# Kernel optimization log

Hardware: AMD Instinct MI355X
Metric: run time of the kernel (lower is better)

Reference implementation:

```python
import jax, jax.numpy as jnp
import numpy as np
import math

R1 = 1.0
R2 = 4.0
NBINS_XY = 4
NBINS_ZY = 4
PARTITIONS = NBINS_XY * NBINS_ZY * 2  # 32
TOPK = 200
TWO_PI = 2.0 * math.pi
PI = math.pi


def setup_inputs() -> dict:
    key = jax.random.key(0)
    k1, k2 = jax.random.split(key)
    # LiDAR-like coordinates, ~[-30, 30] meters
    sampled_vehicle_points = jax.random.normal(k1, (1024, 3), dtype=jnp.float32) * 20.0
    fusion_point = jax.random.normal(k2, (20000, 3), dtype=jnp.float32) * 20.0
    return {"sampled_vehicle_points": sampled_vehicle_points, "fusion_point": fusion_point}


def _compute_partitions_batch(q):
    # q: [S, K, 3]. rel[b, i, j] = q[b, j] - q[b, i]  (A.unsqueeze(1) - B.unsqueeze(2))
    rel = q[:, None, :, :] - q[:, :, None, :]  # [S, K, K, 3]
    angles_xy = jnp.fmod(jnp.arctan2(rel[..., 1], rel[..., 0]) + TWO_PI, TWO_PI)
    angles_zy = jnp.fmod(jnp.arctan2(rel[..., 1], rel[..., 2]) + TWO_PI, PI)
    xy_bins = jnp.floor(angles_xy / (TWO_PI / NBINS_XY))
    zy_bins = jnp.floor(angles_zy / (PI / NBINS_ZY))
    # hash(A, B, seed=NBINS_ZY): -1 where either < 0
    angle_ok = (xy_bins >= 0) & (zy_bins >= 0)
    angles_bins = jnp.where(angle_ok, xy_bins * NBINS_ZY + zy_bins, -1.0)
    D = jnp.sqrt(jnp.sum(rel * rel, axis=-1) + 1e-7)  # [S, K, K]
    dist_bins = jnp.where(D >= R2, 1.0, jnp.where(D >= R1, 0.0, -1.0))
    bin_ok = (dist_bins >= 0) & (angles_bins >= 0)
    bins = jnp.where(bin_ok, dist_bins * (NBINS_XY * NBINS_ZY) + angles_bins, -1.0)
    return bins  # [S, K, K] float, -1 for ignored


def reference(sampled_vehicle_points, fusion_point):
    # kNN query: K nearest fusion points for each sampled vehicle point
    d2 = jnp.sum(
        (sampled_vehicle_points[:, None, :] - fusion_point[None, :, :]) ** 2, axis=-1
    )  # [S, Nf]
    _, idx = jax.lax.top_k(-d2, TOPK)  # indices of TOPK smallest distances
    queried = fusion_point[idx]  # [S, K, 3]

    bins = _compute_partitions_batch(queried)  # [S, K, K]
    row0 = bins[:, 0, :]  # [S, K] — only row 0 is used by the loss
    # points_in_partition[s, p] = sum_j (row0[s, j] == p) + 1
    counts = jnp.sum(
        row0[:, :, None] == jnp.arange(PARTITIONS, dtype=bins.dtype)[None, None, :],
        axis=1,
    ).astype(jnp.float32) + 1.0  # [S, P]
    pip = counts / jnp.linalg.norm(counts, axis=-1, keepdims=True) * 4.0
    gt_dist = jax.nn.softmax(pip, axis=-1)
    return gt_dist
```

## Files before the change

kernel.cpp:

```cpp
#include <hip/hip_runtime.h>
#include <math.h>

#define KTOP 200
#define NPART 32
#define BLOCK 512
#define NHIST 2048
#define CAND_CAP 512
#define WCAP 512
#define CLIST_CAP 1536
#define SRANK_MIN 64u

__device__ __forceinline__ float d2_ref(float ax, float ay, float az,
                                        float bx, float by, float bz) {
    float dx = __fsub_rn(ax, bx), dy = __fsub_rn(ay, by), dz = __fsub_rn(az, bz);
    return __fadd_rn(__fadd_rn(__fmul_rn(dx, dx), __fmul_rn(dy, dy)), __fmul_rn(dz, dz));
}

__device__ __forceinline__ unsigned key_of(const float* __restrict__ fus, int j,
                                           float vx, float vy, float vz) {
    return __float_as_uint(d2_ref(vx, vy, vz, fus[3*j], fus[3*j+1], fus[3*j+2]));
}

__device__ __forceinline__ int compute_bin(float rx, float ry, float rz) {
    const float TWO_PI_F = (float)6.283185307179586;
    const float PI_F     = (float)3.141592653589793;
    const float XY_W     = (float)(6.283185307179586 / 4.0);
    const float ZY_W     = (float)(3.141592653589793 / 4.0);

    float d2 = __fadd_rn(__fadd_rn(__fmul_rn(rx, rx), __fmul_rn(ry, ry)), __fmul_rn(rz, rz));
    float D  = sqrtf(__fadd_rn(d2, 1e-7f));
    float dist_bin;
    if (D >= 4.0f)      dist_bin = 1.0f;
    else if (D >= 1.0f) dist_bin = 0.0f;
    else                return -1;

    float axy = fmodf(atan2f(ry, rx) + TWO_PI_F, TWO_PI_F);
    float azy = fmodf(atan2f(ry, rz) + TWO_PI_F, PI_F);
    float xyb = floorf(__fdiv_rn(axy, XY_W));
    float zyb = floorf(__fdiv_rn(azy, ZY_W));
    if (!(xyb >= 0.0f && zyb >= 0.0f)) return -1;
    float ab  = xyb * 4.0f + zyb;
    int bin = (int)(dist_bin * 16.0f + ab);
    return bin;
}

__global__ __launch_bounds__(BLOCK, 8)
void shape_context_kernel(const float* __restrict__ veh,
                          const float* __restrict__ fus,
                          float* __restrict__ out,
                          int nfus) {
    const int b   = blockIdx.x;
    const int tid = threadIdx.x;
    const int lane = tid & 63;
    const int wid  = tid >> 6;

    __shared__ unsigned int hist[NHIST];
    __shared__ unsigned long long clist[CLIST_CAP];
    __shared__ unsigned long long cand[CAND_CAP];
    __shared__ int wlist[WCAP];
    __shared__ unsigned int hist32[NPART];
    __shared__ unsigned int waveTot[BLOCK / 64];
    __shared__ unsigned int waveBase[BLOCK / 64];
    __shared__ unsigned int s_bucket, s_rem, s_bcount;
    __shared__ int s_candCount, s_wcount, s_clistCount;
    __shared__ float s_q0[3];
    __shared__ unsigned long long s_minPacked, s_lowBound;

    const float vx = veh[b * 3 + 0], vy = veh[b * 3 + 1], vz = veh[b * 3 + 2];
    const float4* fus4 = (const float4*)fus;
    const int ntrip = nfus >> 2;

    if (tid == 0) { s_minPacked = ~0ull; s_candCount = 0; s_wcount = 0; s_clistCount = 0; }
    for (int i = tid; i < NHIST; i += BLOCK) hist[i] = 0;
    if (tid < NPART) hist32[tid] = 0;
    __syncthreads();

    auto find_bucket = [&](unsigned remq) {
        if (tid == 0) s_bucket = 0xFFFFFFFFu;
        const int PER = NHIST / BLOCK;
        int base = tid * PER;
        unsigned p = 0;
        #pragma unroll
        for (int i = 0; i < PER; i++) p += hist[base + i];
        unsigned incl = p;
        #pragma unroll
        for (int d = 1; d < 64; d <<= 1) {
            unsigned n = __shfl_up(incl, d, 64);
            if (lane >= d) incl += n;
        }
        if (lane == 63) waveTot[wid] = incl;
        __syncthreads();
        if (tid == 0) {
            unsigned acc = 0;
            for (int w = 0; w < BLOCK / 64; w++) { waveBase[w] = acc; acc += waveTot[w]; }
        }
        __syncthreads();
        unsigned excl = waveBase[wid] + incl - p;
        if (excl < remq && remq <= excl + p) {
            unsigned cum = excl;
            #pragma unroll
            for (int i = 0; i < PER; i++) {
                unsigned c = hist[base + i];
                if (cum + c >= remq) { s_bucket = base + i; s_rem = remq - cum; s_bcount = c; break; }
                cum += c;
            }
        }
        __syncthreads();
    };

    auto push_l = [&](unsigned k, unsigned j) {
        int pos = atomicAdd(&s_clistCount, 1);
        if (pos < CLIST_CAP) clist[pos] = ((unsigned long long)k << 32) | j;
    };

    unsigned k0 = 0, k1 = 0, k2 = 0, k3 = 0;
    const bool t0v = (tid < ntrip);
    if (t0v) {
        float4 A = fus4[3 * tid], Bq = fus4[3 * tid + 1], Cq = fus4[3 * tid + 2];
        k0 = __float_as_uint(d2_ref(vx, vy, vz, A.x,  A.y,  A.z));
        k1 = __float_as_uint(d2_ref(vx, vy, vz, A.w,  Bq.x, Bq.y));
        k2 = __float_as_uint(d2_ref(vx, vy, vz, Bq.z, Bq.w, Cq.x));
        k3 = __float_as_uint(d2_ref(vx, vy, vz, Cq.y, Cq.z, Cq.w));
        atomicAdd(&hist[k0 >> 21], 1u);
        atomicAdd(&hist[k1 >> 21], 1u);
        atomicAdd(&hist[k2 >> 21], 1u);
        atomicAdd(&hist[k3 >> 21], 1u);
    }
    __syncthreads();

    unsigned srank;
    {
        long long sample = (long long)((ntrip < BLOCK) ? ntrip : BLOCK) * 4;
        if (sample >= (long long)nfus) {
            srank = KTOP;
        } else {
            unsigned s2 = (unsigned)(((long long)3 * KTOP * sample + nfus - 1) / nfus);
            srank = (s2 < SRANK_MIN) ? SRANK_MIN : s2;
        }
    }
    find_bucket(srank);
    const unsigned E = (s_bucket < NHIST) ? s_bucket : (NHIST - 1);
    const unsigned maxKey = ((E + 1u) << 21) - 1u;

    if (t0v) {
        unsigned jb = 4u * (unsigned)tid;
        if (k0 <= maxKey) push_l(k0, jb + 0);
        if (k1 <= maxKey) push_l(k1, jb + 1);
        if (k2 <= maxKey) push_l(k2, jb + 2);
        if (k3 <= maxKey) push_l(k3, jb + 3);
    }

    {
        int m = BLOCK + tid;
        bool valid = (m < ntrip);
        float4 A, Bq, Cq;
        if (valid) { A = fus4[3 * m]; Bq = fus4[3 * m + 1]; Cq = fus4[3 * m + 2]; }
        while (valid) {
            const int mn = m + BLOCK;
            const bool vnext = (mn < ntrip);
            float4 An, Bn, Cn;
            if (vnext) { An = fus4[3 * mn]; Bn = fus4[3 * mn + 1]; Cn = fus4[3 * mn + 2]; }

            unsigned q0k = __float_as_uint(d2_ref(vx, vy, vz, A.x,  A.y,  A.z));
            unsigned q1k = __float_as_uint(d2_ref(vx, vy, vz, A.w,  Bq.x, Bq.y));
            unsigned q2k = __float_as_uint(d2_ref(vx, vy, vz, Bq.z, Bq.w, Cq.x));
            unsigned q3k = __float_as_uint(d2_ref(vx, vy, vz, Cq.y, Cq.z, Cq.w));
            unsigned long long m0 = __ballot(q0k <= maxKey);
            unsigned long long m1 = __ballot(q1k <= maxKey);
            unsigned long long m2 = __ballot(q2k <= maxKey);
            unsigned long long m3 = __ballot(q3k <= maxKey);
            if (m0 | m1 | m2 | m3) {
                int c0 = __popcll(m0), c1 = __popcll(m1), c2 = __popcll(m2);
                int tot = c0 + c1 + c2 + __popcll(m3);
                int base = 0;
                if (lane == 0) base = atomicAdd(&s_clistCount, tot);
                base = __shfl(base, 0, 64);
                const unsigned long long lt = (1ull << lane) - 1ull;
                unsigned jb = 4u * (unsigned)m;
                int o0 = base + (int)__popcll(m0 & lt);
                int o1 = base + c0 + (int)__popcll(m1 & lt);
                int o2 = base + c0 + c1 + (int)__popcll(m2 & lt);
                int o3 = base + c0 + c1 + c2 + (int)__popcll(m3 & lt);
                if (q0k <= maxKey && o0 < CLIST_CAP) clist[o0] = ((unsigned long long)q0k << 32) | (jb + 0);
                if (q1k <= maxKey && o1 < CLIST_CAP) clist[o1] = ((unsigned long long)q1k << 32) | (jb + 1);
                if (q2k <= maxKey && o2 < CLIST_CAP) clist[o2] = ((unsigned long long)q2k << 32) | (jb + 2);
                if (q3k <= maxKey && o3 < CLIST_CAP) clist[o3] = ((unsigned long long)q3k << 32) | (jb + 3);
            }
            A = An; Bq = Bn; Cq = Cn; m = mn; valid = vnext;
        }
    }
    for (int j = (nfus & ~3) + tid; j < nfus; j += BLOCK) {
        unsigned k = key_of(fus, j, vx, vy, vz);
        if (k <= maxKey) push_l(k, (unsigned)j);
    }
    __syncthreads();

    const int cnRaw = s_clistCount;
    const bool noOvf = (cnRaw <= CLIST_CAP);
    if (noOvf) {
        for (int i = tid; i <= (int)E; i += BLOCK) hist[i] = 0;
        __syncthreads();
        for (int i = tid; i < cnRaw; i += BLOCK)
            atomicAdd(&hist[(unsigned)(clist[i] >> 53)], 1u);
        __syncthreads();
    }

    find_bucket(KTOP);
    unsigned T = s_bucket;
    unsigned rem = s_rem;
    unsigned bcount = s_bcount;
    int shift = 21;
    const bool fastOK = noOvf && (T <= E);

    if (fastOK) {
        unsigned long long lm = ~0ull;
        for (int i = tid; i < cnRaw; i += BLOCK) { unsigned long long p = clist[i]; lm = (p < lm) ? p : lm; }
        #pragma unroll
        for (int d = 32; d > 0; d >>= 1) {
            unsigned long long o = __shfl_xor(lm, d, 64);
            lm = (o < lm) ? o : lm;
        }
        if (lane == 0) atomicMin(&s_minPacked, lm);
        __syncthreads();
    } else {
        for (int i = tid; i < NHIST; i += BLOCK) hist[i] = 0;
        __syncthreads();
        unsigned long long lm = ~0ull;
        for (int j = tid; j < nfus; j += BLOCK) {
            unsigned k = key_of(fus, j, vx, vy, vz);
            atomicAdd(&hist[k >> 21], 1u);
            unsigned long long p = ((unsigned long long)k << 32) | (unsigned)j;
            lm = (p < lm) ? p : lm;
        }
        #pragma unroll
        for (int d = 32; d > 0; d >>= 1) {
            unsigned long long o = __shfl_xor(lm, d, 64);
            lm = (o < lm) ? o : lm;
        }
        if (lane == 0) atomicMin(&s_minPacked, lm);
        __syncthreads();
        find_bucket(KTOP);
        T = s_bucket; rem = s_rem; bcount = s_bcount;
    }

    if (tid == 0) {
        int idx0 = (int)(s_minPacked & 0xFFFFFFFFull);
        s_q0[0] = fus[idx0 * 3]; s_q0[1] = fus[idx0 * 3 + 1]; s_q0[2] = fus[idx0 * 3 + 2];
    }
    __syncthreads();
    const float q0x = s_q0[0], q0y = s_q0[1], q0z = s_q0[2];

    while (bcount > CAND_CAP && shift > 0) {
        int newshift = (shift > 11) ? (shift - 11) : 0;
        unsigned digmask = (1u << (shift - newshift)) - 1;
        for (int i = tid; i < NHIST; i += BLOCK) hist[i] = 0;
        __syncthreads();
        for (int j = tid; j < nfus; j += BLOCK) {
            unsigned k = key_of(fus, j, vx, vy, vz);
            if ((k >> shift) == T) atomicAdd(&hist[(k >> newshift) & digmask], 1u);
        }
        __syncthreads();
        find_bucket(rem);
        T = (T << (shift - newshift)) | s_bucket;
        rem = s_rem;
        bcount = s_bcount;
        shift = newshift;
    }

    if (fastOK && shift == 21) {
        for (int i = tid; i < cnRaw; i += BLOCK) {
            unsigned long long p = clist[i];
            unsigned hi = (unsigned)(p >> 53);
            if (hi < T) {
                int pos = atomicAdd(&s_wcount, 1);
                if (pos < WCAP) wlist[pos] = (int)(p & 0xFFFFFFFFull);
            } else if (hi == T) {
                int pos = atomicAdd(&s_candCount, 1);
                if (pos < CAND_CAP) cand[pos] = p;
            }
        }
    } else {
        for (int j = tid; j < nfus; j += BLOCK) {
            unsigned k = key_of(fus, j, vx, vy, vz);
            unsigned hi = k >> shift;
            if (hi < T) { int pos = atomicAdd(&s_wcount, 1); if (pos < WCAP) wlist[pos] = j; }
            else if (hi == T) { int pos = atomicAdd(&s_candCount, 1); if (pos < CAND_CAP) cand[pos] = ((unsigned long long)k << 32) | (unsigned)j; }
        }
    }
    __syncthreads();

    const int cnt = s_candCount;
    if (cnt <= CAND_CAP) {
        for (int i = tid; i < cnt; i += BLOCK) {
            unsigned long long me = cand[i];
            int rank = 0;
            for (int k2 = 0; k2 < cnt; k2++) rank += (cand[k2] < me) ? 1 : 0;
            if (rank < (int)rem) {
                int pos = atomicAdd(&s_wcount, 1);
                if (pos < WCAP) wlist[pos] = (int)(me & 0xFFFFFFFFull);
            }
        }
    }
    __syncthreads();

    {
        int wc = s_wcount; if (wc > WCAP) wc = WCAP;
        for (int i = tid; i < wc; i += BLOCK) {
            int j = wlist[i];
            float fx = fus[3 * j], fy = fus[3 * j + 1], fz = fus[3 * j + 2];
            int bin = compute_bin(__fsub_rn(fx, q0x), __fsub_rn(fy, q0y), __fsub_rn(fz, q0z));
            if (bin >= 0 && bin < NPART) atomicAdd(&hist32[bin], 1u);
        }
    }
    __syncthreads();

    if (cnt > CAND_CAP) {
        if (tid == 0) s_lowBound = 0;
        __syncthreads();
        for (unsigned itx = 0; itx < rem; ++itx) {
            if (tid == 0) s_minPacked = ~0ull;
            __syncthreads();
            unsigned long long lowB = s_lowBound;
            unsigned long long lm = ~0ull;
            for (int j = tid; j < nfus; j += BLOCK) {
                unsigned k = key_of(fus, j, vx, vy, vz);
                if ((k >> shift) == T) {
                    unsigned long long p = ((unsigned long long)k << 32) | (unsigned)j;
                    if (p >= lowB && p < lm) lm = p;
                }
            }
            #pragma unroll
            for (int d = 32; d > 0; d >>= 1) {
                unsigned long long o = __shfl_xor(lm, d, 64);
                lm = (o < lm) ? o : lm;
            }
            if (lane == 0) atomicMin(&s_minPacked, lm);
            __syncthreads();
            if (tid == 0) {
                int jm = (int)(s_minPacked & 0xFFFFFFFFull);
                float fx = fus[jm * 3], fy = fus[jm * 3 + 1], fz = fus[jm * 3 + 2];
                int bin = compute_bin(__fsub_rn(fx, q0x), __fsub_rn(fy, q0y), __fsub_rn(fz, q0z));
                if (bin >= 0 && bin < NPART) hist32[bin] += 1u;
                s_lowBound = s_minPacked + 1;
            }
            __syncthreads();
        }
    }

    if (tid < NPART) {
        float c = (float)hist32[tid] + 1.0f;
        float ss = __fmul_rn(c, c);
        #pragma unroll
        for (int d = 16; d > 0; d >>= 1) ss += __shfl_xor(ss, d, 64);
        float v = __fmul_rn(__fdiv_rn(c, sqrtf(ss)), 4.0f);
        float mx = v;
        #pragma unroll
        for (int d = 16; d > 0; d >>= 1) mx = fmaxf(mx, __shfl_xor(mx, d, 64));
        float e = expf(v - mx);
        float sum = e;
        #pragma unroll
        for (int d = 16; d > 0; d >>= 1) sum += __shfl_xor(sum, d, 64);
        out[b * NPART + tid] = __fdiv_rn(e, sum);
    }
}

extern "C" void kernel_launch(void* const* d_in, const int* in_sizes, int n_in,
                              void* d_out, int out_size, void* d_ws, size_t ws_size,
                              hipStream_t stream) {
    const float* veh = (const float*)d_in[0];
    const float* fus = (const float*)d_in[1];
    float* out = (float*)d_out;
    int nveh = in_sizes[0] / 3;
    int nfus = in_sizes[1] / 3;
    shape_context_kernel<<<nveh, BLOCK, 0, stream>>>(veh, fus, out, nfus);
}
```

Measured before the change: 77.23 us.

## Split kNN shape-context kernel into planarize, sample, chunked filter, select stages

The single fused per-query kernel is replaced by a four-kernel pipeline when workspace is available. Fusion points are converted to SoA, and a per-query threshold is estimated from a fixed sample. The full distance filter is split across 8 chunks per query so more blocks share the streaming work, with wave-aggregated ballot appends into a global candidate list. A final per-query kernel does the exact selection and binning. This spreads the dominant streaming pass over more CUs, at the cost of extra launches and global-memory round trips for the candidate lists.

```diff
diff --git a/kernel.cpp b/kernel.cpp
--- a/kernel.cpp
+++ b/kernel.cpp
@@ -3,17 +3,27 @@
 
 #define KTOP 200
 #define NPART 32
-#define BLOCK 512
 #define NHIST 2048
 #define CAND_CAP 512
 #define WCAP 512
 #define CLIST_CAP 1536
 #define SRANK_MIN 64u
+#define NCHUNK 8
+#define K0B 256
+#define K1B 256
+#define K2B 512
+#define BLOCK 512
+#define SAMPLE_MAX 2048
 
 __device__ __forceinline__ float d2_ref(float ax, float ay, float az,
                                         float bx, float by, float bz) {
     float dx = __fsub_rn(ax, bx), dy = __fsub_rn(ay, by), dz = __fsub_rn(az, bz);
     return __fadd_rn(__fadd_rn(__fmul_rn(dx, dx), __fmul_rn(dy, dy)), __fmul_rn(dz, dz));
+}
+
+__device__ __forceinline__ unsigned key2(float cx, float cy, float cz,
+                                         float px, float py, float pz) {
+    return __float_as_uint(d2_ref(cx, cy, cz, px, py, pz));
 }
 
 __device__ __forceinline__ unsigned key_of(const float* __restrict__ fus, int j,
@@ -44,11 +54,340 @@
     return bin;
 }
 
+template<int B>
+__device__ __forceinline__ void find_bucket_dev(const unsigned* __restrict__ hist,
+                                                unsigned remq,
+                                                unsigned* waveTot, unsigned* waveBase,
+                                                unsigned* s_bucket, unsigned* s_rem,
+                                                unsigned* s_bcount, int tid) {
+    const int lane = tid & 63, wid = tid >> 6;
+    if (tid == 0) *s_bucket = 0xFFFFFFFFu;
+    const int PER = NHIST / B;
+    int base = tid * PER;
+    unsigned p = 0;
+    #pragma unroll
+    for (int i = 0; i < PER; i++) p += hist[base + i];
+    unsigned incl = p;
+    #pragma unroll
+    for (int d = 1; d < 64; d <<= 1) {
+        unsigned n = __shfl_up(incl, d, 64);
+        if (lane >= d) incl += n;
+    }
+    if (lane == 63) waveTot[wid] = incl;
+    __syncthreads();
+    if (tid == 0) {
+        unsigned acc = 0;
+        for (int w = 0; w < B / 64; w++) { waveBase[w] = acc; acc += waveTot[w]; }
+    }
+    __syncthreads();
+    unsigned excl = waveBase[wid] + incl - p;
+    if (excl < remq && remq <= excl + p) {
+        unsigned cum = excl;
+        #pragma unroll
+        for (int i = 0; i < PER; i++) {
+            unsigned c = hist[base + i];
+            if (cum + c >= remq) { *s_bucket = base + i; *s_rem = remq - cum; *s_bcount = c; break; }
+            cum += c;
+        }
+    }
+    __syncthreads();
+}
+
+__global__ void planarize_kernel(const float* __restrict__ fus,
+                                 float* __restrict__ fx, float* __restrict__ fy,
+                                 float* __restrict__ fz, int nfus, int padN) {
+    int j = blockIdx.x * blockDim.x + threadIdx.x;
+    if (j < nfus) {
+        fx[j] = fus[3*j]; fy[j] = fus[3*j+1]; fz[j] = fus[3*j+2];
+    } else if (j < padN) {
+        fx[j] = 0.f; fy[j] = 0.f; fz[j] = 0.f;
+    }
+}
+
+__global__ __launch_bounds__(K0B, 8)
+void sample_bound_kernel(const float* __restrict__ veh,
+                         const float* __restrict__ fx, const float* __restrict__ fy,
+                         const float* __restrict__ fz,
+                         unsigned* __restrict__ mk, int* __restrict__ cnt, int nfus) {
+    const int v = blockIdx.x;
+    const int tid = threadIdx.x;
+    __shared__ unsigned hist[NHIST];
+    __shared__ unsigned waveTot[K0B/64], waveBase[K0B/64];
+    __shared__ unsigned s_bucket, s_rem, s_bcount;
+
+    const float vx = veh[v*3], vy = veh[v*3+1], vz = veh[v*3+2];
+    for (int i = tid; i < NHIST; i += K0B) hist[i] = 0;
+    __syncthreads();
+    const int S = (nfus < SAMPLE_MAX) ? nfus : SAMPLE_MAX;
+    for (int j = tid; j < S; j += K0B) {
+        unsigned k = key2(vx, vy, vz, fx[j], fy[j], fz[j]);
+        atomicAdd(&hist[k >> 21], 1u);
+    }
+    __syncthreads();
+    unsigned srank;
+    if (S >= nfus) srank = KTOP;
+    else {
+        unsigned s2 = (unsigned)((3LL * KTOP * S + nfus - 1) / nfus);
+        srank = (s2 < SRANK_MIN) ? SRANK_MIN : s2;
+    }
+    find_bucket_dev<K0B>(hist, srank, waveTot, waveBase, &s_bucket, &s_rem, &s_bcount, tid);
+    if (tid == 0) {
+        unsigned e = (s_bucket < NHIST) ? s_bucket : (NHIST - 1);
+        mk[v] = ((e + 1u) << 21) - 1u;
+        cnt[v] = 0;
+    }
+}
+
+__global__ __launch_bounds__(K1B, 8)
+void stream_filter_kernel(const float* __restrict__ veh,
+                          const float4* __restrict__ fx4, const float4* __restrict__ fy4,
+                          const float4* __restrict__ fz4,
+                          const unsigned* __restrict__ mk, int* __restrict__ cnt,
+                          unsigned long long* __restrict__ clG, int nfus, int ppc) {
+    const int bx = blockIdx.x;
+    const int v  = bx / NCHUNK;
+    const int c  = bx - v * NCHUNK;
+    const int tid = threadIdx.x;
+    const int lane = tid & 63;
+    const float vx = veh[v*3], vy = veh[v*3+1], vz = veh[v*3+2];
+    const unsigned maxKey = mk[v];
+    unsigned long long* cl = clG + (size_t)v * CLIST_CAP;
+    int* cp = cnt + v;
+    const int pbase = c * ppc;
+    int pend = pbase + ppc; if (pend > nfus) pend = nfus;
+
+    for (int p4 = (pbase >> 2) + tid; (p4 << 2) < pend; p4 += K1B) {
+        const int j0 = p4 << 2;
+        float4 X = fx4[p4], Y = fy4[p4], Z = fz4[p4];
+        unsigned k0 = key2(vx, vy, vz, X.x, Y.x, Z.x);
+        unsigned k1 = key2(vx, vy, vz, X.y, Y.y, Z.y);
+        unsigned k2 = key2(vx, vy, vz, X.z, Y.z, Z.z);
+        unsigned k3 = key2(vx, vy, vz, X.w, Y.w, Z.w);
+        bool q0 = (k0 <= maxKey);
+        bool q1 = (k1 <= maxKey) && (j0 + 1 < pend);
+        bool q2 = (k2 <= maxKey) && (j0 + 2 < pend);
+        bool q3 = (k3 <= maxKey) && (j0 + 3 < pend);
+        unsigned long long m0 = __ballot(q0), m1 = __ballot(q1);
+        unsigned long long m2 = __ballot(q2), m3 = __ballot(q3);
+        if (m0 | m1 | m2 | m3) {
+            int c0 = __popcll(m0), c1 = __popcll(m1), c2 = __popcll(m2);
+            int tot = c0 + c1 + c2 + __popcll(m3);
+            int base = 0;
+            if (lane == 0) base = atomicAdd(cp, tot);
+            base = __shfl(base, 0, 64);
+            const unsigned long long lt = (1ull << lane) - 1ull;
+            int o0 = base + (int)__popcll(m0 & lt);
+            int o1 = base + c0 + (int)__popcll(m1 & lt);
+            int o2 = base + c0 + c1 + (int)__popcll(m2 & lt);
+            int o3 = base + c0 + c1 + c2 + (int)__popcll(m3 & lt);
+            if (q0 && o0 < CLIST_CAP) cl[o0] = ((unsigned long long)k0 << 32) | (unsigned)(j0 + 0);
+            if (q1 && o1 < CLIST_CAP) cl[o1] = ((unsigned long long)k1 << 32) | (unsigned)(j0 + 1);
+            if (q2 && o2 < CLIST_CAP) cl[o2] = ((unsigned long long)k2 << 32) | (unsigned)(j0 + 2);
+            if (q3 && o3 < CLIST_CAP) cl[o3] = ((unsigned long long)k3 << 32) | (unsigned)(j0 + 3);
+        }
+    }
+}
+
+__global__ __launch_bounds__(K2B, 8)
+void select_bin_kernel(const float* __restrict__ veh,
+                       const float* __restrict__ fx, const float* __restrict__ fy,
+                       const float* __restrict__ fz,
+                       const unsigned* __restrict__ mk, const int* __restrict__ cntArr,
+                       const unsigned long long* __restrict__ clG,
+                       float* __restrict__ out, int nfus) {
+    const int v = blockIdx.x;
+    const int tid = threadIdx.x;
+    const int lane = tid & 63;
+
+    __shared__ unsigned hist[NHIST];
+    __shared__ unsigned long long clistS[CLIST_CAP];
+    __shared__ unsigned long long cand[CAND_CAP];
+    __shared__ int wlist[WCAP];
+    __shared__ unsigned hist32[NPART];
+    __shared__ unsigned waveTot[K2B/64], waveBase[K2B/64];
+    __shared__ unsigned s_bucket, s_rem, s_bcount;
+    __shared__ int s_candCount, s_wcount;
+    __shared__ float s_q0[3];
+    __shared__ unsigned long long s_minPacked, s_lowBound;
+
+    const float vx = veh[v*3], vy = veh[v*3+1], vz = veh[v*3+2];
+    const unsigned maxKey = mk[v];
+    const unsigned E = maxKey >> 21;
+    const int cnRaw = cntArr[v];
+    const bool noOvf = (cnRaw <= CLIST_CAP);
+    const int cn = noOvf ? cnRaw : CLIST_CAP;
+    const unsigned long long* clg = clG + (size_t)v * CLIST_CAP;
+
+    if (tid == 0) { s_minPacked = ~0ull; s_candCount = 0; s_wcount = 0; }
+    if (tid < NPART) hist32[tid] = 0;
+    for (int i = tid; i < NHIST; i += K2B) hist[i] = 0;
+    for (int i = tid; i < cn; i += K2B) clistS[i] = clg[i];
+    __syncthreads();
+    if (noOvf) {
+        for (int i = tid; i < cn; i += K2B) atomicAdd(&hist[(unsigned)(clistS[i] >> 53)], 1u);
+    }
+    __syncthreads();
+
+    find_bucket_dev<K2B>(hist, KTOP, waveTot, waveBase, &s_bucket, &s_rem, &s_bcount, tid);
+    unsigned T = s_bucket, rem = s_rem, bcount = s_bcount;
+    int shift = 21;
+    const bool fastOK = noOvf && (T <= E);
+
+    if (fastOK) {
+        unsigned long long lm = ~0ull;
+        for (int i = tid; i < cn; i += K2B) { unsigned long long p = clistS[i]; lm = (p < lm) ? p : lm; }
+        #pragma unroll
+        for (int d = 32; d > 0; d >>= 1) {
+            unsigned long long o = __shfl_xor(lm, d, 64);
+            lm = (o < lm) ? o : lm;
+        }
+        if (lane == 0) atomicMin(&s_minPacked, lm);
+        __syncthreads();
+    } else {
+        for (int i = tid; i < NHIST; i += K2B) hist[i] = 0;
+        __syncthreads();
+        unsigned long long lm = ~0ull;
+        for (int j = tid; j < nfus; j += K2B) {
+            unsigned k = key2(vx, vy, vz, fx[j], fy[j], fz[j]);
+            atomicAdd(&hist[k >> 21], 1u);
+            unsigned long long p = ((unsigned long long)k << 32) | (unsigned)j;
+            lm = (p < lm) ? p : lm;
+        }
+        #pragma unroll
+        for (int d = 32; d > 0; d >>= 1) {
+            unsigned long long o = __shfl_xor(lm, d, 64);
+            lm = (o < lm) ? o : lm;
+        }
+        if (lane == 0) atomicMin(&s_minPacked, lm);
+        __syncthreads();
+        find_bucket_dev<K2B>(hist, KTOP, waveTot, waveBase, &s_bucket, &s_rem, &s_bcount, tid);
+        T = s_bucket; rem = s_rem; bcount = s_bcount;
+    }
+
+    if (tid == 0) {
+        int i0 = (int)(s_minPacked & 0xFFFFFFFFull);
+        s_q0[0] = fx[i0]; s_q0[1] = fy[i0]; s_q0[2] = fz[i0];
+    }
+    __syncthreads();
+    const float q0x = s_q0[0], q0y = s_q0[1], q0z = s_q0[2];
+
+    while (bcount > CAND_CAP && shift > 0) {
+        int newshift = (shift > 11) ? (shift - 11) : 0;
+        unsigned digmask = (1u << (shift - newshift)) - 1;
+        for (int i = tid; i < NHIST; i += K2B) hist[i] = 0;
+        __syncthreads();
+        for (int j = tid; j < nfus; j += K2B) {
+            unsigned k = key2(vx, vy, vz, fx[j], fy[j], fz[j]);
+            if ((k >> shift) == T) atomicAdd(&hist[(k >> newshift) & digmask], 1u);
+        }
+        __syncthreads();
+        find_bucket_dev<K2B>(hist, rem, waveTot, waveBase, &s_bucket, &s_rem, &s_bcount, tid);
+        T = (T << (shift - newshift)) | s_bucket;
+        rem = s_rem;
+        bcount = s_bcount;
+        shift = newshift;
+    }
+
+    if (fastOK && shift == 21) {
+        for (int i = tid; i < cn; i += K2B) {
+            unsigned long long p = clistS[i];
+            unsigned hi = (unsigned)(p >> 53);
+            if (hi < T) {
+                int pos = atomicAdd(&s_wcount, 1);
+                if (pos < WCAP) wlist[pos] = (int)(p & 0xFFFFFFFFull);
+            } else if (hi == T) {
+                int pos = atomicAdd(&s_candCount, 1);
+                if (pos < CAND_CAP) cand[pos] = p;
+            }
+        }
+    } else {
+        for (int j = tid; j < nfus; j += K2B) {
+            unsigned k = key2(vx, vy, vz, fx[j], fy[j], fz[j]);
+            unsigned hi = k >> shift;
+            if (hi < T) { int pos = atomicAdd(&s_wcount, 1); if (pos < WCAP) wlist[pos] = j; }
+            else if (hi == T) { int pos = atomicAdd(&s_candCount, 1); if (pos < CAND_CAP) cand[pos] = ((unsigned long long)k << 32) | (unsigned)j; }
+        }
+    }
+    __syncthreads();
+
+    const int cnt2 = s_candCount;
+    if (cnt2 <= CAND_CAP) {
+        for (int i = tid; i < cnt2; i += K2B) {
+            unsigned long long me = cand[i];
+            int rank = 0;
+            for (int k2i = 0; k2i < cnt2; k2i++) rank += (cand[k2i] < me) ? 1 : 0;
+            if (rank < (int)rem) {
+                int pos = atomicAdd(&s_wcount, 1);
+                if (pos < WCAP) wlist[pos] = (int)(me & 0xFFFFFFFFull);
+            }
+        }
+    }
+    __syncthreads();
+
+    {
+        int wc = s_wcount; if (wc > WCAP) wc = WCAP;
+        for (int i = tid; i < wc; i += K2B) {
+            int j = wlist[i];
+            int bin = compute_bin(__fsub_rn(fx[j], q0x), __fsub_rn(fy[j], q0y), __fsub_rn(fz[j], q0z));
+            if (bin >= 0 && bin < NPART) atomicAdd(&hist32[bin], 1u);
+        }
+    }
+    __syncthreads();
+
+    if (cnt2 > CAND_CAP) {
+        if (tid == 0) s_lowBound = 0;
+        __syncthreads();
+        for (unsigned itx = 0; itx < rem; ++itx) {
+            if (tid == 0) s_minPacked = ~0ull;
+            __syncthreads();
+            unsigned long long lowB = s_lowBound;
+            unsigned long long lm = ~0ull;
+            for (int j = tid; j < nfus; j += K2B) {
+                unsigned k = key2(vx, vy, vz, fx[j], fy[j], fz[j]);
+                if ((k >> shift) == T) {
+                    unsigned long long p = ((unsigned long long)k << 32) | (unsigned)j;
+                    if (p >= lowB && p < lm) lm = p;
+                }
+            }
+            #pragma unroll
+            for (int d = 32; d > 0; d >>= 1) {
+                unsigned long long o = __shfl_xor(lm, d, 64);
+                lm = (o < lm) ? o : lm;
+            }
+            if (lane == 0) atomicMin(&s_minPacked, lm);
+            __syncthreads();
+            if (tid == 0) {
+                int jm = (int)(s_minPacked & 0xFFFFFFFFull);
+                int bin = compute_bin(__fsub_rn(fx[jm], q0x), __fsub_rn(fy[jm], q0y), __fsub_rn(fz[jm], q0z));
+                if (bin >= 0 && bin < NPART) hist32[bin] += 1u;
+                s_lowBound = s_minPacked + 1;
+            }
+            __syncthreads();
+        }
+    }
+
+    if (tid < NPART) {
+        float c = (float)hist32[tid] + 1.0f;
+        float ss = __fmul_rn(c, c);
+        #pragma unroll
+        for (int d = 16; d > 0; d >>= 1) ss += __shfl_xor(ss, d, 64);
+        float vv = __fmul_rn(__fdiv_rn(c, sqrtf(ss)), 4.0f);
+        float mx = vv;
+        #pragma unroll
+        for (int d = 16; d > 0; d >>= 1) mx = fmaxf(mx, __shfl_xor(mx, d, 64));
+        float e = expf(vv - mx);
+        float sum = e;
+        #pragma unroll
+        for (int d = 16; d > 0; d >>= 1) sum += __shfl_xor(sum, d, 64);
+        out[v * NPART + tid] = __fdiv_rn(e, sum);
+    }
+}
+
 __global__ __launch_bounds__(BLOCK, 8)
-void shape_context_kernel(const float* __restrict__ veh,
-                          const float* __restrict__ fus,
-                          float* __restrict__ out,
-                          int nfus) {
+void shape_context_mono(const float* __restrict__ veh,
+                        const float* __restrict__ fus,
+                        float* __restrict__ out,
+                        int nfus) {
     const int b   = blockIdx.x;
     const int tid = threadIdx.x;
     const int lane = tid & 63;
@@ -74,39 +413,6 @@
     for (int i = tid; i < NHIST; i += BLOCK) hist[i] = 0;
     if (tid < NPART) hist32[tid] = 0;
     __syncthreads();
-
-    auto find_bucket = [&](unsigned remq) {
-        if (tid == 0) s_bucket = 0xFFFFFFFFu;
-        const int PER = NHIST / BLOCK;
-        int base = tid * PER;
-        unsigned p = 0;
-        #pragma unroll
-        for (int i = 0; i < PER; i++) p += hist[base + i];
-        unsigned incl = p;
-        #pragma unroll
-        for (int d = 1; d < 64; d <<= 1) {
-            unsigned n = __shfl_up(incl, d, 64);
-            if (lane >= d) incl += n;
-        }
-        if (lane == 63) waveTot[wid] = incl;
-        __syncthreads();
-        if (tid == 0) {
-            unsigned acc = 0;
-            for (int w = 0; w < BLOCK / 64; w++) { waveBase[w] = acc; acc += waveTot[w]; }
-        }
-        __syncthreads();
-        unsigned excl = waveBase[wid] + incl - p;
-        if (excl < remq && remq <= excl + p) {
-            unsigned cum = excl;
-            #pragma unroll
-            for (int i = 0; i < PER; i++) {
-                unsigned c = hist[base + i];
-                if (cum + c >= remq) { s_bucket = base + i; s_rem = remq - cum; s_bcount = c; break; }
-                cum += c;
-            }
-        }
-        __syncthreads();
-    };
 
     auto push_l = [&](unsigned k, unsigned j) {
         int pos = atomicAdd(&s_clistCount, 1);
@@ -131,14 +437,13 @@
     unsigned srank;
     {
         long long sample = (long long)((ntrip < BLOCK) ? ntrip : BLOCK) * 4;
-        if (sample >= (long long)nfus) {
-            srank = KTOP;
-        } else {
+        if (sample >= (long long)nfus) srank = KTOP;
+        else {
             unsigned s2 = (unsigned)(((long long)3 * KTOP * sample + nfus - 1) / nfus);
             srank = (s2 < SRANK_MIN) ? SRANK_MIN : s2;
         }
     }
-    find_bucket(srank);
+    find_bucket_dev<BLOCK>(hist, srank, waveTot, waveBase, &s_bucket, &s_rem, &s_bcount, tid);
     const unsigned E = (s_bucket < NHIST) ? s_bucket : (NHIST - 1);
     const unsigned maxKey = ((E + 1u) << 21) - 1u;
 
@@ -205,7 +510,7 @@
         __syncthreads();
     }
 
-    find_bucket(KTOP);
+    find_bucket_dev<BLOCK>(hist, KTOP, waveTot, waveBase, &s_bucket, &s_rem, &s_bcount, tid);
     unsigned T = s_bucket;
     unsigned rem = s_rem;
     unsigned bcount = s_bcount;
@@ -239,7 +544,7 @@
         }
         if (lane == 0) atomicMin(&s_minPacked, lm);
         __syncthreads();
-        find_bucket(KTOP);
+        find_bucket_dev<BLOCK>(hist, KTOP, waveTot, waveBase, &s_bucket, &s_rem, &s_bcount, tid);
         T = s_bucket; rem = s_rem; bcount = s_bcount;
     }
 
@@ -260,7 +565,7 @@
             if ((k >> shift) == T) atomicAdd(&hist[(k >> newshift) & digmask], 1u);
         }
         __syncthreads();
-        find_bucket(rem);
+        find_bucket_dev<BLOCK>(hist, rem, waveTot, waveBase, &s_bucket, &s_rem, &s_bcount, tid);
         T = (T << (shift - newshift)) | s_bucket;
         rem = s_rem;
         bcount = s_bcount;
@@ -294,7 +599,7 @@
         for (int i = tid; i < cnt; i += BLOCK) {
             unsigned long long me = cand[i];
             int rank = 0;
-            for (int k2 = 0; k2 < cnt; k2++) rank += (cand[k2] < me) ? 1 : 0;
+            for (int k2i = 0; k2i < cnt; k2i++) rank += (cand[k2i] < me) ? 1 : 0;
             if (rank < (int)rem) {
                 int pos = atomicAdd(&s_wcount, 1);
                 if (pos < WCAP) wlist[pos] = (int)(me & 0xFFFFFFFFull);
@@ -307,8 +612,8 @@
         int wc = s_wcount; if (wc > WCAP) wc = WCAP;
         for (int i = tid; i < wc; i += BLOCK) {
             int j = wlist[i];
-            float fx = fus[3 * j], fy = fus[3 * j + 1], fz = fus[3 * j + 2];
-            int bin = compute_bin(__fsub_rn(fx, q0x), __fsub_rn(fy, q0y), __fsub_rn(fz, q0z));
+            float fxs = fus[3 * j], fys = fus[3 * j + 1], fzs = fus[3 * j + 2];
+            int bin = compute_bin(__fsub_rn(fxs, q0x), __fsub_rn(fys, q0y), __fsub_rn(fzs, q0z));
             if (bin >= 0 && bin < NPART) atomicAdd(&hist32[bin], 1u);
         }
     }
@@ -338,8 +643,8 @@
             __syncthreads();
             if (tid == 0) {
                 int jm = (int)(s_minPacked & 0xFFFFFFFFull);
-                float fx = fus[jm * 3], fy = fus[jm * 3 + 1], fz = fus[jm * 3 + 2];
-                int bin = compute_bin(__fsub_rn(fx, q0x), __fsub_rn(fy, q0y), __fsub_rn(fz, q0z));
+                float fxs = fus[jm * 3], fys = fus[jm * 3 + 1], fzs = fus[jm * 3 + 2];
+                int bin = compute_bin(__fsub_rn(fxs, q0x), __fsub_rn(fys, q0y), __fsub_rn(fzs, q0z));
                 if (bin >= 0 && bin < NPART) hist32[bin] += 1u;
                 s_lowBound = s_minPacked + 1;
             }
@@ -372,5 +677,34 @@
     float* out = (float*)d_out;
     int nveh = in_sizes[0] / 3;
     int nfus = in_sizes[1] / 3;
-    shape_context_kernel<<<nveh, BLOCK, 0, stream>>>(veh, fus, out, nfus);
-}
+
+    size_t nf4   = (size_t)((nfus + 3) >> 2);
+    size_t PB    = ((nf4 * 16) + 255) & ~(size_t)255;
+    size_t szA   = (((size_t)nveh * 4) + 255) & ~(size_t)255;
+    size_t offMk = 3 * PB;
+    size_t offCnt = offMk + szA;
+    size_t offCl  = offCnt + szA;
+    size_t need   = offCl + (size_t)nveh * CLIST_CAP * 8;
+
+    if (d_ws == nullptr || ws_size < need) {
+        shape_context_mono<<<nveh, BLOCK, 0, stream>>>(veh, fus, out, nfus);
+        return;
+    }
+
+    char* ws = (char*)d_ws;
+    float* fx = (float*)(ws);
+    float* fy = (float*)(ws + PB);
+    float* fz = (float*)(ws + 2 * PB);
+    unsigned* mk = (unsigned*)(ws + offMk);
+    int* cnt = (int*)(ws + offCnt);
+    unsigned long long* cl = (unsigned long long*)(ws + offCl);
+
+    int padN = (int)nf4 * 4;
+    int g0 = (padN + 255) / 256;
+    planarize_kernel<<<g0, 256, 0, stream>>>(fus, fx, fy, fz, nfus, padN);
+    sample_bound_kernel<<<nveh, K0B, 0, stream>>>(veh, fx, fy, fz, mk, cnt, nfus);
+    int ppc = ((nfus + NCHUNK - 1) / NCHUNK + 3) & ~3;
+    stream_filter_kernel<<<nveh * NCHUNK, K1B, 0, stream>>>(
+        veh, (const float4*)fx, (const float4*)fy, (const float4*)fz, mk, cnt, cl, nfus, ppc);
+    select_bin_kernel<<<nveh, K2B, 0, stream>>>(veh, fx, fy, fz, mk, cnt, cl, out, nfus);
+}
```

New measurement: 158.8 us. 106% more time.

## Convert fusion points to planar SoA layout in workspace before main kernel

Applied to the files above, without the earlier changes.

Adds a pre-pass kernel that splits the interleaved xyz fusion point array into three planar x/y/z arrays in the workspace buffer. The main kernel is templated to read these arrays as float4 in the scan loops and in the scalar key_of re-scans, so those scalar accesses become coalesced unit-stride loads instead of stride-3 gathers. This costs an extra kernel launch and a write/read of the point data, and it only takes effect when a large enough workspace is provided; otherwise it falls back to the original path.

```diff
diff --git a/kernel.cpp b/kernel.cpp
--- a/kernel.cpp
+++ b/kernel.cpp
@@ -16,6 +16,11 @@
     return __fadd_rn(__fadd_rn(__fmul_rn(dx, dx), __fmul_rn(dy, dy)), __fmul_rn(dz, dz));
 }
 
+__device__ __forceinline__ unsigned key2(float cx, float cy, float cz,
+                                         float px, float py, float pz) {
+    return __float_as_uint(d2_ref(cx, cy, cz, px, py, pz));
+}
+
 __device__ __forceinline__ unsigned key_of(const float* __restrict__ fus, int j,
                                            float vx, float vy, float vz) {
     return __float_as_uint(d2_ref(vx, vy, vz, fus[3*j], fus[3*j+1], fus[3*j+2]));
@@ -44,9 +49,26 @@
     return bin;
 }
 
+__global__ void planarize_kernel(const float* __restrict__ fus,
+                                 float* __restrict__ fx, float* __restrict__ fy,
+                                 float* __restrict__ fz, int nfus) {
+    const int n3 = 3 * nfus;
+    for (int t = blockIdx.x * blockDim.x + threadIdx.x; t < n3; t += gridDim.x * blockDim.x) {
+        float val = fus[t];
+        int p = t / 3;
+        int d = t - 3 * p;
+        float* dst = (d == 0) ? fx : ((d == 1) ? fy : fz);
+        dst[p] = val;
+    }
+}
+
+template<bool PLANAR>
 __global__ __launch_bounds__(BLOCK, 8)
 void shape_context_kernel(const float* __restrict__ veh,
                           const float* __restrict__ fus,
+                          const float* __restrict__ fxp,
+                          const float* __restrict__ fyp,
+                          const float* __restrict__ fzp,
                           float* __restrict__ out,
                           int nfus) {
     const int b   = blockIdx.x;
@@ -68,6 +90,9 @@
 
     const float vx = veh[b * 3 + 0], vy = veh[b * 3 + 1], vz = veh[b * 3 + 2];
     const float4* fus4 = (const float4*)fus;
+    const float4* fx4 = (const float4*)fxp;
+    const float4* fy4 = (const float4*)fyp;
+    const float4* fz4 = (const float4*)fzp;
     const int ntrip = nfus >> 2;
 
     if (tid == 0) { s_minPacked = ~0ull; s_candCount = 0; s_wcount = 0; s_clistCount = 0; }
@@ -113,14 +138,27 @@
         if (pos < CLIST_CAP) clist[pos] = ((unsigned long long)k << 32) | j;
     };
 
+    auto key_j = [&](int j) {
+        if constexpr (PLANAR) return key2(vx, vy, vz, fxp[j], fyp[j], fzp[j]);
+        else                  return key_of(fus, j, vx, vy, vz);
+    };
+
     unsigned k0 = 0, k1 = 0, k2 = 0, k3 = 0;
     const bool t0v = (tid < ntrip);
     if (t0v) {
-        float4 A = fus4[3 * tid], Bq = fus4[3 * tid + 1], Cq = fus4[3 * tid + 2];
-        k0 = __float_as_uint(d2_ref(vx, vy, vz, A.x,  A.y,  A.z));
-        k1 = __float_as_uint(d2_ref(vx, vy, vz, A.w,  Bq.x, Bq.y));
-        k2 = __float_as_uint(d2_ref(vx, vy, vz, Bq.z, Bq.w, Cq.x));
-        k3 = __float_as_uint(d2_ref(vx, vy, vz, Cq.y, Cq.z, Cq.w));
+        if constexpr (PLANAR) {
+            float4 X = fx4[tid], Y = fy4[tid], Z = fz4[tid];
+            k0 = key2(vx, vy, vz, X.x, Y.x, Z.x);
+            k1 = key2(vx, vy, vz, X.y, Y.y, Z.y);
+            k2 = key2(vx, vy, vz, X.z, Y.z, Z.z);
+            k3 = key2(vx, vy, vz, X.w, Y.w, Z.w);
+        } else {
+            float4 A = fus4[3 * tid], Bq = fus4[3 * tid + 1], Cq = fus4[3 * tid + 2];
+            k0 = key2(vx, vy, vz, A.x,  A.y,  A.z);
+            k1 = key2(vx, vy, vz, A.w,  Bq.x, Bq.y);
+            k2 = key2(vx, vy, vz, Bq.z, Bq.w, Cq.x);
+            k3 = key2(vx, vy, vz, Cq.y, Cq.z, Cq.w);
+        }
         atomicAdd(&hist[k0 >> 21], 1u);
         atomicAdd(&hist[k1 >> 21], 1u);
         atomicAdd(&hist[k2 >> 21], 1u);
@@ -154,17 +192,31 @@
         int m = BLOCK + tid;
         bool valid = (m < ntrip);
         float4 A, Bq, Cq;
-        if (valid) { A = fus4[3 * m]; Bq = fus4[3 * m + 1]; Cq = fus4[3 * m + 2]; }
+        if (valid) {
+            if constexpr (PLANAR) { A = fx4[m]; Bq = fy4[m]; Cq = fz4[m]; }
+            else                  { A = fus4[3 * m]; Bq = fus4[3 * m + 1]; Cq = fus4[3 * m + 2]; }
+        }
         while (valid) {
             const int mn = m + BLOCK;
             const bool vnext = (mn < ntrip);
             float4 An, Bn, Cn;
-            if (vnext) { An = fus4[3 * mn]; Bn = fus4[3 * mn + 1]; Cn = fus4[3 * mn + 2]; }
-
-            unsigned q0k = __float_as_uint(d2_ref(vx, vy, vz, A.x,  A.y,  A.z));
-            unsigned q1k = __float_as_uint(d2_ref(vx, vy, vz, A.w,  Bq.x, Bq.y));
-            unsigned q2k = __float_as_uint(d2_ref(vx, vy, vz, Bq.z, Bq.w, Cq.x));
-            unsigned q3k = __float_as_uint(d2_ref(vx, vy, vz, Cq.y, Cq.z, Cq.w));
+            if (vnext) {
+                if constexpr (PLANAR) { An = fx4[mn]; Bn = fy4[mn]; Cn = fz4[mn]; }
+                else                  { An = fus4[3 * mn]; Bn = fus4[3 * mn + 1]; Cn = fus4[3 * mn + 2]; }
+            }
+
+            unsigned q0k, q1k, q2k, q3k;
+            if constexpr (PLANAR) {
+                q0k = key2(vx, vy, vz, A.x, Bq.x, Cq.x);
+                q1k = key2(vx, vy, vz, A.y, Bq.y, Cq.y);
+                q2k = key2(vx, vy, vz, A.z, Bq.z, Cq.z);
+                q3k = key2(vx, vy, vz, A.w, Bq.w, Cq.w);
+            } else {
+                q0k = key2(vx, vy, vz, A.x,  A.y,  A.z);
+                q1k = key2(vx, vy, vz, A.w,  Bq.x, Bq.y);
+                q2k = key2(vx, vy, vz, Bq.z, Bq.w, Cq.x);
+                q3k = key2(vx, vy, vz, Cq.y, Cq.z, Cq.w);
+            }
             unsigned long long m0 = __ballot(q0k <= maxKey);
             unsigned long long m1 = __ballot(q1k <= maxKey);
             unsigned long long m2 = __ballot(q2k <= maxKey);
@@ -190,7 +242,7 @@
         }
     }
     for (int j = (nfus & ~3) + tid; j < nfus; j += BLOCK) {
-        unsigned k = key_of(fus, j, vx, vy, vz);
+        unsigned k = key_j(j);
         if (k <= maxKey) push_l(k, (unsigned)j);
     }
     __syncthreads();
@@ -227,7 +279,7 @@
         __syncthreads();
         unsigned long long lm = ~0ull;
         for (int j = tid; j < nfus; j += BLOCK) {
-            unsigned k = key_of(fus, j, vx, vy, vz);
+            unsigned k = key_j(j);
             atomicAdd(&hist[k >> 21], 1u);
             unsigned long long p = ((unsigned long long)k << 32) | (unsigned)j;
             lm = (p < lm) ? p : lm;
@@ -245,7 +297,8 @@
 
     if (tid == 0) {
         int idx0 = (int)(s_minPacked & 0xFFFFFFFFull);
-        s_q0[0] = fus[idx0 * 3]; s_q0[1] = fus[idx0 * 3 + 1]; s_q0[2] = fus[idx0 * 3 + 2];
+        if constexpr (PLANAR) { s_q0[0] = fxp[idx0]; s_q0[1] = fyp[idx0]; s_q0[2] = fzp[idx0]; }
+        else { s_q0[0] = fus[idx0 * 3]; s_q0[1] = fus[idx0 * 3 + 1]; s_q0[2] = fus[idx0 * 3 + 2]; }
     }
     __syncthreads();
     const float q0x = s_q0[0], q0y = s_q0[1], q0z = s_q0[2];
@@ -256,7 +309,7 @@
         for (int i = tid; i < NHIST; i += BLOCK) hist[i] = 0;
         __syncthreads();
         for (int j = tid; j < nfus; j += BLOCK) {
-            unsigned k = key_of(fus, j, vx, vy, vz);
+            unsigned k = key_j(j);
             if ((k >> shift) == T) atomicAdd(&hist[(k >> newshift) & digmask], 1u);
         }
         __syncthreads();
@@ -281,7 +334,7 @@
         }
     } else {
         for (int j = tid; j < nfus; j += BLOCK) {
-            unsigned k = key_of(fus, j, vx, vy, vz);
+            unsigned k = key_j(j);
             unsigned hi = k >> shift;
             if (hi < T) { int pos = atomicAdd(&s_wcount, 1); if (pos < WCAP) wlist[pos] = j; }
             else if (hi == T) { int pos = atomicAdd(&s_candCount, 1); if (pos < CAND_CAP) cand[pos] = ((unsigned long long)k << 32) | (unsigned)j; }
@@ -294,7 +347,7 @@
         for (int i = tid; i < cnt; i += BLOCK) {
             unsigned long long me = cand[i];
             int rank = 0;
-            for (int k2 = 0; k2 < cnt; k2++) rank += (cand[k2] < me) ? 1 : 0;
+            for (int k2i = 0; k2i < cnt; k2i++) rank += (cand[k2i] < me) ? 1 : 0;
             if (rank < (int)rem) {
                 int pos = atomicAdd(&s_wcount, 1);
                 if (pos < WCAP) wlist[pos] = (int)(me & 0xFFFFFFFFull);
@@ -307,8 +360,10 @@
         int wc = s_wcount; if (wc > WCAP) wc = WCAP;
         for (int i = tid; i < wc; i += BLOCK) {
             int j = wlist[i];
-            float fx = fus[3 * j], fy = fus[3 * j + 1], fz = fus[3 * j + 2];
-            int bin = compute_bin(__fsub_rn(fx, q0x), __fsub_rn(fy, q0y), __fsub_rn(fz, q0z));
+            float fxs, fys, fzs;
+            if constexpr (PLANAR) { fxs = fxp[j]; fys = fyp[j]; fzs = fzp[j]; }
+            else { fxs = fus[3 * j]; fys = fus[3 * j + 1]; fzs = fus[3 * j + 2]; }
+            int bin = compute_bin(__fsub_rn(fxs, q0x), __fsub_rn(fys, q0y), __fsub_rn(fzs, q0z));
             if (bin >= 0 && bin < NPART) atomicAdd(&hist32[bin], 1u);
         }
     }
@@ -323,7 +378,7 @@
             unsigned long long lowB = s_lowBound;
             unsigned long long lm = ~0ull;
             for (int j = tid; j < nfus; j += BLOCK) {
-                unsigned k = key_of(fus, j, vx, vy, vz);
+                unsigned k = key_j(j);
                 if ((k >> shift) == T) {
                     unsigned long long p = ((unsigned long long)k << 32) | (unsigned)j;
                     if (p >= lowB && p < lm) lm = p;
@@ -338,8 +393,10 @@
             __syncthreads();
             if (tid == 0) {
                 int jm = (int)(s_minPacked & 0xFFFFFFFFull);
-                float fx = fus[jm * 3], fy = fus[jm * 3 + 1], fz = fus[jm * 3 + 2];
-                int bin = compute_bin(__fsub_rn(fx, q0x), __fsub_rn(fy, q0y), __fsub_rn(fz, q0z));
+                float fxs, fys, fzs;
+                if constexpr (PLANAR) { fxs = fxp[jm]; fys = fyp[jm]; fzs = fzp[jm]; }
+                else { fxs = fus[3 * jm]; fys = fus[3 * jm + 1]; fzs = fus[3 * jm + 2]; }
+                int bin = compute_bin(__fsub_rn(fxs, q0x), __fsub_rn(fys, q0y), __fsub_rn(fzs, q0z));
                 if (bin >= 0 && bin < NPART) hist32[bin] += 1u;
                 s_lowBound = s_minPacked + 1;
             }
@@ -372,5 +429,21 @@
     float* out = (float*)d_out;
     int nveh = in_sizes[0] / 3;
     int nfus = in_sizes[1] / 3;
-    shape_context_kernel<<<nveh, BLOCK, 0, stream>>>(veh, fus, out, nfus);
-}
+
+    size_t nf4 = (size_t)((nfus + 3) >> 2);
+    size_t PB  = ((nf4 * 16) + 255) & ~(size_t)255;
+    size_t need = 3 * PB;
+
+    if (d_ws != nullptr && ws_size >= need) {
+        char* ws = (char*)d_ws;
+        float* fx = (float*)(ws);
+        float* fy = (float*)(ws + PB);
+        float* fz = (float*)(ws + 2 * PB);
+        int g0 = (3 * nfus + 255) / 256;
+        planarize_kernel<<<g0, 256, 0, stream>>>(fus, fx, fy, fz, nfus);
+        shape_context_kernel<true><<<nveh, BLOCK, 0, stream>>>(veh, fus, fx, fy, fz, out, nfus);
+    } else {
+        shape_context_kernel<false><<<nveh, BLOCK, 0, stream>>>(
+            veh, fus, nullptr, nullptr, nullptr, out, nfus);
+    }
+}
```

Measured after the change: 79.19 us. +2.5%, slower.
